# Performance work log

Measured on AMD Instinct MI355X. Metric: run time of the kernel, lower is better.

Reference implementation:

```python
import jax, jax.numpy as jnp
import numpy as np

B, N, F_IN = 2, 2048, 256
HEADS, F_OUT = 8, 32
NEG_SLOPE = 0.01  # torch F.leaky_relu default


def setup_inputs() -> dict:
    key = jax.random.key(0)
    k1, k2, k3, k4 = jax.random.split(key, 4)
    stdv = 1.0 / np.sqrt(F_OUT * HEADS)
    h = jax.random.normal(k1, (B, N, F_IN), dtype=jnp.float32)
    adj = jax.random.uniform(k2, (B, N, N), dtype=jnp.float32)
    W = jax.random.normal(k3, (F_IN, F_OUT * HEADS), dtype=jnp.float32) * stdv
    a = jax.random.normal(k4, (2 * F_OUT, 1), dtype=jnp.float32) * stdv
    return {"h": h, "adj": adj, "W": W, "a": a}


def reference(h, adj, W, a):
    # adj is accepted by the original forward but never used (dense attention).
    b, n, _ = h.shape
    f = a.shape[0] // 2
    heads = W.shape[1] // f
    Wh = (h @ W).reshape(b, n, heads, f)            # [b,n,h,f]
    a1 = a[:f, 0]                                    # attends to source i
    a2 = a[f:, 0]                                    # attends to target j
    e1 = jnp.einsum('bnhf,f->bhn', Wh, a1)           # [b,h,n]
    e2 = jnp.einsum('bnhf,f->bhn', Wh, a2)           # [b,h,n]
    # e[b,h,i,j] = leaky_relu(a1.Wh_i + a2.Wh_j) == a^T [Wh_i || Wh_j]
    e = jax.nn.leaky_relu(e1[:, :, :, None] + e2[:, :, None, :], NEG_SLOPE)
    att = jax.nn.softmax(e, axis=-1)                 # softmax over neighbors j
    h_prime = jnp.einsum('bhij,bjhf->bihf', att, Wh)  # [b,n,h,f]
    return h_prime.reshape(b, n, heads * f)
```

## Files before the change

kernel.cpp:

```cpp
#include <hip/hip_runtime.h>
#include <math.h>

#define BATCH 2
#define NTOK  2048
#define FIN   256
#define HEADS 8
#define FOUT  32
#define BH    (BATCH*HEADS)
#define NCOL  (HEADS*FOUT)
#define ROWS  (BATCH*NTOK)

typedef _Float16 f16;
typedef _Float16 f16x8 __attribute__((ext_vector_type(8)));
typedef float    f32x4 __attribute__((ext_vector_type(4)));

static const size_t OFF_E1   = 1048576;
static const size_t OFF_E2   = OFF_E1 + 32768;
static const size_t OFF_SKEY = OFF_E2 + 32768;
static const size_t OFF_SIDX = OFF_SKEY + 32768;
static const size_t OFF_W1S  = OFF_SIDX + 32768;
static const size_t OFF_W2S  = OFF_W1S + 32768;
static const size_t OFF_S1   = OFF_W2S + 32768;
static const size_t OFF_P2   = OFF_S1 + 32784;
static const size_t OFF_V1   = OFF_P2 + 32784;
static const size_t OFF_P2V  = OFF_V1 + 16u*2049u*32u;
static const size_t OFF_HHI  = OFF_P2V + 16u*2049u*32u;
static const size_t OFF_HLO  = OFF_HHI + 524288;
static const size_t OFF_WTHI = OFF_HLO + 524288;
static const size_t OFF_WTLO = OFF_WTHI + 32768;

__global__ __launch_bounds__(256) void k_split(const float* __restrict__ h,
                                               const float* __restrict__ W,
                                               f16* __restrict__ hhi, f16* __restrict__ hlo,
                                               f16* __restrict__ wthi, f16* __restrict__ wtlo) {
    const int tid = threadIdx.x;
    if (blockIdx.x < 512) {
        const size_t base = ((size_t)blockIdx.x * 256 + tid) * 8;
        const float4 v0 = *(const float4*)(h + base);
        const float4 v1 = *(const float4*)(h + base + 4);
        const float xs[8] = {v0.x,v0.y,v0.z,v0.w,v1.x,v1.y,v1.z,v1.w};
        f16x8 hi8, lo8;
        #pragma unroll
        for (int i = 0; i < 8; ++i) {
            float xv = xs[i] * 16.0f;
            f16 hv = (f16)xv;
            hi8[i] = hv;
            lo8[i] = (f16)(xv - (float)hv);
        }
        *(f16x8*)(hhi + base) = hi8;
        *(f16x8*)(hlo + base) = lo8;
    } else {
        const int k0 = (blockIdx.x - 512) * 16;
        const int c  = tid;
        f16x8 hiA, loA, hiB, loB;
        #pragma unroll
        for (int j = 0; j < 8; ++j) {
            float xv = W[(size_t)(k0 + j) * 256 + c] * 4096.0f;
            f16 hv = (f16)xv;
            hiA[j] = hv; loA[j] = (f16)(xv - (float)hv);
        }
        #pragma unroll
        for (int j = 0; j < 8; ++j) {
            float xv = W[(size_t)(k0 + 8 + j) * 256 + c] * 4096.0f;
            f16 hv = (f16)xv;
            hiB[j] = hv; loB[j] = (f16)(xv - (float)hv);
        }
        f16* pd = wthi + (size_t)c * 256 + k0;
        f16* pe = wtlo + (size_t)c * 256 + k0;
        *(f16x8*)pd = hiA; *(f16x8*)(pd + 8) = hiB;
        *(f16x8*)pe = loA; *(f16x8*)(pe + 8) = loB;
    }
}

__global__ __launch_bounds__(256) void k_mm(const f16* __restrict__ hhi, const f16* __restrict__ hlo,
                                            const f16* __restrict__ wthi, const f16* __restrict__ wtlo,
                                            const float* __restrict__ a,
                                            float* __restrict__ Wh,
                                            float* __restrict__ e1, float* __restrict__ e2) {
    const int tid  = threadIdx.x;
    const int wv   = tid >> 6;
    const int lane = tid & 63;
    const int r    = lane & 15;
    const int q    = lane >> 4;
    const int row0 = blockIdx.x * 16;
    const int col0 = wv * 64;
    const int koff = q * 8;

    const f16* pa_hi = hhi  + (size_t)(row0 + r) * 256 + koff;
    const f16* pa_lo = hlo  + (size_t)(row0 + r) * 256 + koff;
    const f16* pb_hi = wthi + (size_t)(col0 + r) * 256 + koff;
    const f16* pb_lo = wtlo + (size_t)(col0 + r) * 256 + koff;

    f32x4 acc[4];
    #pragma unroll
    for (int t = 0; t < 4; ++t) acc[t] = (f32x4){0.f,0.f,0.f,0.f};

    struct FR { f16x8 ah, al, bh[4], bl[4]; };
    auto ldfr = [&](int ch) {
        FR f;
        const int o = ch * 32;
        f.ah = *(const f16x8*)(pa_hi + o);
        f.al = *(const f16x8*)(pa_lo + o);
        #pragma unroll
        for (int t = 0; t < 4; ++t) {
            f.bh[t] = *(const f16x8*)(pb_hi + t * (16 * 256) + o);
            f.bl[t] = *(const f16x8*)(pb_lo + t * (16 * 256) + o);
        }
        return f;
    };
    auto dom = [&](const FR& f) {
        #pragma unroll
        for (int t = 0; t < 4; ++t) {
            acc[t] = __builtin_amdgcn_mfma_f32_16x16x32_f16(f.ah, f.bh[t], acc[t], 0, 0, 0);
            acc[t] = __builtin_amdgcn_mfma_f32_16x16x32_f16(f.ah, f.bl[t], acc[t], 0, 0, 0);
            acc[t] = __builtin_amdgcn_mfma_f32_16x16x32_f16(f.al, f.bh[t], acc[t], 0, 0, 0);
        }
    };

    FR fa = ldfr(0);
    FR fb = ldfr(1);
    #pragma unroll
    for (int ch = 0; ch < 8; ch += 2) {
        dom(fa);
        if (ch + 2 < 8) fa = ldfr(ch + 2);
        dom(fb);
        if (ch + 3 < 8) fb = ldfr(ch + 3);
    }

    const float SC = 1.0f / 65536.0f;
    #pragma unroll
    for (int t = 0; t < 4; ++t) acc[t] *= SC;

    #pragma unroll
    for (int t = 0; t < 4; ++t)
        #pragma unroll
        for (int g = 0; g < 4; ++g)
            Wh[(size_t)(row0 + q * 4 + g) * 256 + col0 + t * 16 + r] = acc[t][g];

    const float av10 = a[r], av11 = a[16 + r], av20 = a[32 + r], av21 = a[48 + r];
    float p1[8], p2[8];
    #pragma unroll
    for (int hp = 0; hp < 2; ++hp)
        #pragma unroll
        for (int g = 0; g < 4; ++g) {
            p1[hp * 4 + g] = acc[2 * hp][g] * av10 + acc[2 * hp + 1][g] * av11;
            p2[hp * 4 + g] = acc[2 * hp][g] * av20 + acc[2 * hp + 1][g] * av21;
        }
    #pragma unroll
    for (int m = 1; m < 16; m <<= 1) {
        #pragma unroll
        for (int i = 0; i < 8; ++i) {
            p1[i] += __shfl_xor(p1[i], m, 64);
            p2[i] += __shfl_xor(p2[i], m, 64);
        }
    }
    if (r == 0) {
        #pragma unroll
        for (int hp = 0; hp < 2; ++hp)
            #pragma unroll
            for (int g = 0; g < 4; ++g) {
                const int row  = row0 + q * 4 + g;
                const int b    = row >> 11;
                const int n    = row & (NTOK - 1);
                const int head = wv * 2 + hp;
                e1[(b * HEADS + head) * NTOK + n] = p1[hp * 4 + g];
                e2[(b * HEADS + head) * NTOK + n] = p2[hp * 4 + g];
            }
    }
}

__device__ __forceinline__ unsigned long long sortkey(float f, int j) {
    unsigned int b = __float_as_uint(f);
    unsigned int u = (b & 0x80000000u) ? ~b : (b | 0x80000000u);
    return ((unsigned long long)u << 32) | (unsigned int)(NTOK - 1 - j);
}

__global__ __launch_bounds__(512) void k_rank(const float* __restrict__ e2g,
                                              float* __restrict__ skey, int* __restrict__ sidx,
                                              float* __restrict__ w1s, float* __restrict__ w2s) {
    __shared__ unsigned long long keys[NTOK];
    __shared__ int prank[2][256];
    const int tid = threadIdx.x;
    const int bh  = blockIdx.x;
    const int jt  = blockIdx.y;
    #pragma unroll
    for (int qq = 0; qq < 4; ++qq) {
        int idx = qq * 512 + tid;
        keys[idx] = sortkey(e2g[bh * NTOK + idx], idx);
    }
    __syncthreads();
    const int jl = tid & 255;
    const int hf = tid >> 8;
    const int j  = jt * 256 + jl;
    const unsigned long long my = keys[j];
    int rank = 0;
    const ulonglong2* c2 = (const ulonglong2*)(keys + hf * 1024);
    #pragma unroll 8
    for (int qq = 0; qq < 512; ++qq) {
        ulonglong2 v = c2[qq];
        rank += (v.x > my);
        rank += (v.y > my);
    }
    prank[hf][jl] = rank;
    __syncthreads();
    if (tid < 256) {
        const int rk = prank[0][tid] + prank[1][tid];
        const int jj = jt * 256 + tid;
        const float myf = e2g[bh * NTOK + jj];
        skey[bh * NTOK + rk] = myf;
        sidx[bh * NTOK + rk] = jj;
        w1s[bh * NTOK + rk]  = expf(myf);
        w2s[bh * NTOK + rk]  = expf(0.01f * myf);
    }
}

__global__ __launch_bounds__(1024) void k_vscan(const float* __restrict__ Wh,
                                                const int* __restrict__ sidx,
                                                const float* __restrict__ w1s,
                                                const float* __restrict__ w2s,
                                                float* __restrict__ V1,
                                                float* __restrict__ P2V,
                                                float* __restrict__ S1,
                                                float* __restrict__ P2) {
    __shared__ float4 wtot[16];
    __shared__ float4 woff[16];
    const int t    = threadIdx.x;
    const int lane = t & 63;
    const int wv   = t >> 6;
    const int fg   = blockIdx.x;
    const int bh   = blockIdx.y;
    const int z    = blockIdx.z;
    const int b    = bh >> 3;
    const int hh   = bh & 7;
    const float* wsrc = z ? w2s : w1s;

    const int j0 = 2 * t;
    float4 v0, v1;
    if (fg < 8) {
        int sj0 = sidx[bh * NTOK + j0];
        int sj1 = sidx[bh * NTOK + j0 + 1];
        float w0 = wsrc[bh * NTOK + j0];
        float w1 = wsrc[bh * NTOK + j0 + 1];
        float4 g0 = *(const float4*)(Wh + (size_t)(b * NTOK + sj0) * NCOL + hh * FOUT + fg * 4);
        float4 g1 = *(const float4*)(Wh + (size_t)(b * NTOK + sj1) * NCOL + hh * FOUT + fg * 4);
        v0 = make_float4(w0 * g0.x, w0 * g0.y, w0 * g0.z, w0 * g0.w);
        v1 = make_float4(w1 * g1.x, w1 * g1.y, w1 * g1.z, w1 * g1.w);
    } else {
        v0 = make_float4(wsrc[bh * NTOK + j0],     0.f, 0.f, 0.f);
        v1 = make_float4(wsrc[bh * NTOK + j0 + 1], 0.f, 0.f, 0.f);
    }

    float4 s = make_float4(v0.x + v1.x, v0.y + v1.y, v0.z + v1.z, v0.w + v1.w);
    #pragma unroll
    for (int d = 1; d < 64; d <<= 1) {
        float ux = __shfl_up(s.x, (unsigned)d, 64);
        float uy = __shfl_up(s.y, (unsigned)d, 64);
        float uz = __shfl_up(s.z, (unsigned)d, 64);
        float uw = __shfl_up(s.w, (unsigned)d, 64);
        if (lane >= d) { s.x += ux; s.y += uy; s.z += uz; s.w += uw; }
    }
    float4 pair = make_float4(v0.x + v1.x, v0.y + v1.y, v0.z + v1.z, v0.w + v1.w);
    float4 excl = make_float4(s.x - pair.x, s.y - pair.y, s.z - pair.z, s.w - pair.w);
    if (lane == 63) wtot[wv] = s;
    __syncthreads();
    if (t < 16) {
        float4 ws = wtot[t];
        float4 inc = ws;
        #pragma unroll
        for (int d = 1; d < 16; d <<= 1) {
            float ux = __shfl_up(inc.x, (unsigned)d, 16);
            float uy = __shfl_up(inc.y, (unsigned)d, 16);
            float uz = __shfl_up(inc.z, (unsigned)d, 16);
            float uw = __shfl_up(inc.w, (unsigned)d, 16);
            if ((t & 15) >= d) { inc.x += ux; inc.y += uy; inc.z += uz; inc.w += uw; }
        }
        woff[t] = make_float4(inc.x - ws.x, inc.y - ws.y, inc.z - ws.z, inc.w - ws.w);
    }
    __syncthreads();

    float4 base = woff[wv];
    float4 i0 = make_float4(base.x + excl.x + v0.x, base.y + excl.y + v0.y,
                            base.z + excl.z + v0.z, base.w + excl.w + v0.w);
    float4 i1 = make_float4(i0.x + v1.x, i0.y + v1.y, i0.z + v1.z, i0.w + v1.w);

    if (fg < 8) {
        float* dst = z ? P2V : V1;
        float* plane = dst + ((size_t)bh * 8 + fg) * (2049u * 4u);
        *(float4*)(plane + (size_t)(j0 + 1) * 4) = i0;
        *(float4*)(plane + (size_t)(j0 + 2) * 4) = i1;
        if (t == 0)
            *(float4*)plane = make_float4(0.f,0.f,0.f,0.f);
    } else {
        float* dst = z ? P2 : S1;
        dst[bh * 2049 + j0 + 1] = i0.x;
        dst[bh * 2049 + j0 + 2] = i1.x;
        if (t == 0) dst[bh * 2049] = 0.f;
    }
}

__global__ __launch_bounds__(256) void k_out(const float* __restrict__ skey,
                                             const float* __restrict__ e1g,
                                             const float* __restrict__ S1,
                                             const float* __restrict__ P2,
                                             const float* __restrict__ V1,
                                             const float* __restrict__ P2V,
                                             float* __restrict__ out) {
    __shared__ float keys[NTOK];
    const int tid = threadIdx.x;
    const int it  = blockIdx.x;
    const int bh  = blockIdx.y;
    const int b   = bh >> 3;
    const int hh  = bh & 7;
    #pragma unroll
    for (int q = 0; q < 8; ++q)
        keys[q * 256 + tid] = skey[bh * NTOK + q * 256 + tid];
    __syncthreads();

    const int i  = it * 32 + (tid >> 3);
    const int fg = tid & 7;
    const float e1v = e1g[bh * NTOK + i];
    const float th  = -e1v;
    int lo = 0, hi = NTOK;
    while (lo < hi) {
        int mid = (lo + hi) >> 1;
        if (keys[mid] > th) lo = mid + 1; else hi = mid;
    }
    const int k = lo;
    const float A = expf(e1v);
    const float C = expf(0.01f * e1v);
    const float s1  = S1[bh * 2049 + k];
    const float p2k = P2[bh * 2049 + k];
    const float p2t = P2[bh * 2049 + 2048];
    const float l   = A * s1 + C * (p2t - p2k);
    const float inv = 1.0f / l;
    const float* v1p  = V1  + ((size_t)bh * 8 + fg) * (2049u * 4u);
    const float* p2vp = P2V + ((size_t)bh * 8 + fg) * (2049u * 4u);
    float4 v1   = *(const float4*)(v1p  + (size_t)k * 4);
    float4 p2v  = *(const float4*)(p2vp + (size_t)k * 4);
    float4 p2vt = *(const float4*)(p2vp + (size_t)2048 * 4);
    float4 o;
    o.x = (A * v1.x + C * (p2vt.x - p2v.x)) * inv;
    o.y = (A * v1.y + C * (p2vt.y - p2v.y)) * inv;
    o.z = (A * v1.z + C * (p2vt.z - p2v.z)) * inv;
    o.w = (A * v1.w + C * (p2vt.w - p2v.w)) * inv;
    *(float4*)(out + (size_t)(b * NTOK + i) * NCOL + hh * FOUT + fg * 4) = o;
}

extern "C" void kernel_launch(void* const* d_in, const int* in_sizes, int n_in,
                              void* d_out, int out_size, void* d_ws, size_t ws_size,
                              hipStream_t stream) {
    const float* h = (const float*)d_in[0];
    const float* W = (const float*)d_in[2];
    const float* a = (const float*)d_in[3];
    float* out = (float*)d_out;
    float* ws  = (float*)d_ws;

    float* Wh   = ws;
    float* e1   = ws + OFF_E1;
    float* e2   = ws + OFF_E2;
    float* skey = ws + OFF_SKEY;
    int*   sidx = (int*)(ws + OFF_SIDX);
    float* w1s  = ws + OFF_W1S;
    float* w2s  = ws + OFF_W2S;
    float* S1   = ws + OFF_S1;
    float* P2   = ws + OFF_P2;
    float* V1   = ws + OFF_V1;
    float* P2V  = ws + OFF_P2V;
    f16*   hhi  = (f16*)(ws + OFF_HHI);
    f16*   hlo  = (f16*)(ws + OFF_HLO);
    f16*   wthi = (f16*)(ws + OFF_WTHI);
    f16*   wtlo = (f16*)(ws + OFF_WTLO);

    k_split<<<528,            256, 0, stream>>>(h, W, hhi, hlo, wthi, wtlo);
    k_mm   <<<256,            256, 0, stream>>>(hhi, hlo, wthi, wtlo, a, Wh, e1, e2);
    k_rank <<<dim3(BH, 8),    512, 0, stream>>>(e2, skey, sidx, w1s, w2s);
    k_vscan<<<dim3(9, BH, 2),1024, 0, stream>>>(Wh, sidx, w1s, w2s, V1, P2V, S1, P2);
    k_out  <<<dim3(NTOK/32, BH), 256, 0, stream>>>(skey, e1, S1, P2, V1, P2V, out);
}
```

Baseline: 131.0 us.

## Split rank-sort counting across key chunks and add separate scatter kernel

The counting-based rank computation is split over a third grid dimension of 8 key chunks. Each block now loads only 256 keys into shared memory and writes a partial rank to a workspace buffer, and a new scatter kernel sums the 8 partials and writes the sorted arrays. The goal is more parallel blocks and less per-block shared-memory loading and serial comparison work. The cost is an extra kernel launch and a global round trip for the partial ranks. The partial buffer reuses the V1 region, which is only written later by k_vscan.

After: 124.1 us. 1.06x faster.

```diff
diff --git a/kernel.cpp b/kernel.cpp
--- a/kernel.cpp
+++ b/kernel.cpp
@@ -28,6 +28,7 @@
 static const size_t OFF_HLO  = OFF_HHI + 524288;
 static const size_t OFF_WTHI = OFF_HLO + 524288;
 static const size_t OFF_WTLO = OFF_WTHI + 32768;
+static const size_t OFF_PART = OFF_V1;
 
 __global__ __launch_bounds__(256) void k_split(const float* __restrict__ h,
                                                const float* __restrict__ W,
@@ -175,43 +176,49 @@
     return ((unsigned long long)u << 32) | (unsigned int)(NTOK - 1 - j);
 }
 
-__global__ __launch_bounds__(512) void k_rank(const float* __restrict__ e2g,
-                                              float* __restrict__ skey, int* __restrict__ sidx,
-                                              float* __restrict__ w1s, float* __restrict__ w2s) {
-    __shared__ unsigned long long keys[NTOK];
-    __shared__ int prank[2][256];
+__global__ __launch_bounds__(256) void k_rank8(const float* __restrict__ e2g,
+                                               int* __restrict__ partial) {
+    __shared__ alignas(16) unsigned long long ch[256];
     const int tid = threadIdx.x;
     const int bh  = blockIdx.x;
     const int jt  = blockIdx.y;
-    #pragma unroll
-    for (int qq = 0; qq < 4; ++qq) {
-        int idx = qq * 512 + tid;
-        keys[idx] = sortkey(e2g[bh * NTOK + idx], idx);
-    }
+    const int kt  = blockIdx.z;
+    const int kbase = kt * 256;
+    ch[tid] = sortkey(e2g[bh * NTOK + kbase + tid], kbase + tid);
     __syncthreads();
-    const int jl = tid & 255;
-    const int hf = tid >> 8;
-    const int j  = jt * 256 + jl;
-    const unsigned long long my = keys[j];
+
+    const int j = jt * 256 + tid;
+    const unsigned long long my = sortkey(e2g[bh * NTOK + j], j);
     int rank = 0;
-    const ulonglong2* c2 = (const ulonglong2*)(keys + hf * 1024);
+    const ulonglong2* c2 = (const ulonglong2*)ch;
     #pragma unroll 8
-    for (int qq = 0; qq < 512; ++qq) {
-        ulonglong2 v = c2[qq];
+    for (int q = 0; q < 128; ++q) {
+        ulonglong2 v = c2[q];
         rank += (v.x > my);
         rank += (v.y > my);
     }
-    prank[hf][jl] = rank;
-    __syncthreads();
-    if (tid < 256) {
-        const int rk = prank[0][tid] + prank[1][tid];
-        const int jj = jt * 256 + tid;
-        const float myf = e2g[bh * NTOK + jj];
-        skey[bh * NTOK + rk] = myf;
-        sidx[bh * NTOK + rk] = jj;
-        w1s[bh * NTOK + rk]  = expf(myf);
-        w2s[bh * NTOK + rk]  = expf(0.01f * myf);
-    }
+    partial[(kt * BH + bh) * NTOK + j] = rank;
+}
+
+__global__ __launch_bounds__(256) void k_scatter(const float* __restrict__ e2g,
+                                                 const int* __restrict__ partial,
+                                                 float* __restrict__ skey,
+                                                 int* __restrict__ sidx,
+                                                 float* __restrict__ w1s,
+                                                 float* __restrict__ w2s) {
+    const int tid = threadIdx.x;
+    const int bh  = blockIdx.x;
+    const int jt  = blockIdx.y;
+    const int j   = jt * 256 + tid;
+    int rank = 0;
+    #pragma unroll
+    for (int kt = 0; kt < 8; ++kt)
+        rank += partial[(kt * BH + bh) * NTOK + j];
+    const float my = e2g[bh * NTOK + j];
+    skey[bh * NTOK + rank] = my;
+    sidx[bh * NTOK + rank] = j;
+    w1s[bh * NTOK + rank]  = expf(my);
+    w2s[bh * NTOK + rank]  = expf(0.01f * my);
 }
 
 __global__ __launch_bounds__(1024) void k_vscan(const float* __restrict__ Wh,
@@ -370,10 +377,12 @@
     f16*   hlo  = (f16*)(ws + OFF_HLO);
     f16*   wthi = (f16*)(ws + OFF_WTHI);
     f16*   wtlo = (f16*)(ws + OFF_WTLO);
-
-    k_split<<<528,            256, 0, stream>>>(h, W, hhi, hlo, wthi, wtlo);
-    k_mm   <<<256,            256, 0, stream>>>(hhi, hlo, wthi, wtlo, a, Wh, e1, e2);
-    k_rank <<<dim3(BH, 8),    512, 0, stream>>>(e2, skey, sidx, w1s, w2s);
-    k_vscan<<<dim3(9, BH, 2),1024, 0, stream>>>(Wh, sidx, w1s, w2s, V1, P2V, S1, P2);
-    k_out  <<<dim3(NTOK/32, BH), 256, 0, stream>>>(skey, e1, S1, P2, V1, P2V, out);
-}
+    int*   part = (int*)(ws + OFF_PART);
+
+    k_split  <<<528,              256, 0, stream>>>(h, W, hhi, hlo, wthi, wtlo);
+    k_mm     <<<256,              256, 0, stream>>>(hhi, hlo, wthi, wtlo, a, Wh, e1, e2);
+    k_rank8  <<<dim3(BH, 8, 8),   256, 0, stream>>>(e2, part);
+    k_scatter<<<dim3(BH, 8),      256, 0, stream>>>(e2, part, skey, sidx, w1s, w2s);
+    k_vscan  <<<dim3(9, BH, 2),  1024, 0, stream>>>(Wh, sidx, w1s, w2s, V1, P2V, S1, P2);
+    k_out    <<<dim3(NTOK/32, BH),256, 0, stream>>>(skey, e1, S1, P2, V1, P2V, out);
+}
```
